# Optimization experiments

Measured on AMD Instinct MI355X. Metric: run time of the kernel, lower is better.

The kernel has to match this reference:

```python
import jax, jax.numpy as jnp
import numpy as np

DIM = 192
WIN = 7
HEADS = 6
SHIFT = 3
HID = 4 * DIM


def _ln(x, w, b, eps=1e-5):
    m = jnp.mean(x, axis=-1, keepdims=True)
    v = jnp.var(x, axis=-1, keepdims=True)
    return (x - m) * jax.lax.rsqrt(v + eps) * w + b


def setup_inputs() -> dict:
    key = jax.random.key(0)
    ks = jax.random.split(key, 8)
    B, C, H, W = 16, DIM, 56, 56
    s = lambda k, shape, fan: jax.random.normal(k, shape, jnp.float32) * (1.0 / np.sqrt(fan))
    return {
        "x": jax.random.normal(ks[0], (B, C, H, W), jnp.float32),
        "norm1_w": jnp.ones((C,), jnp.float32),
        "norm1_b": jnp.zeros((C,), jnp.float32),
        "qkv_w": s(ks[1], (3 * C, C), C),
        "qkv_b": jnp.zeros((3 * C,), jnp.float32),
        "proj_w": s(ks[2], (C, C), C),
        "proj_b": jnp.zeros((C,), jnp.float32),
        "norm2_w": jnp.ones((C,), jnp.float32),
        "norm2_b": jnp.zeros((C,), jnp.float32),
        "fc1_w": s(ks[3], (HID, C), C),
        "fc1_b": jnp.zeros((HID,), jnp.float32),
        "fc2_w": s(ks[4], (C, HID), HID),
        "fc2_b": jnp.zeros((C,), jnp.float32),
    }


def reference(x, norm1_w, norm1_b, qkv_w, qkv_b, proj_w, proj_b,
              norm2_w, norm2_b, fc1_w, fc1_b, fc2_w, fc2_b):
    B, C, H, W = x.shape
    shift = SHIFT if (H > WIN and W > WIN) else 0
    shortcut = x

    xl = jnp.transpose(x, (0, 2, 3, 1))            # B,H,W,C
    xl = _ln(xl, norm1_w, norm1_b)
    if shift > 0:
        xl = jnp.roll(xl, shift=(-shift, -shift), axis=(1, 2))
    nH, nW = H // WIN, W // WIN
    xw = xl.reshape(B, nH, WIN, nW, WIN, C)
    xw = jnp.transpose(xw, (0, 1, 3, 2, 4, 5)).reshape(-1, WIN * WIN, C)

    # window attention
    Bw, N, _ = xw.shape
    dh = C // HEADS
    qkv = jnp.einsum('bnc,oc->bno', xw, qkv_w) + qkv_b
    qkv = qkv.reshape(Bw, N, 3, HEADS, dh)
    q, k, v = qkv[:, :, 0], qkv[:, :, 1], qkv[:, :, 2]   # Bw,N,H,dh
    scale = dh ** -0.5
    attn = jnp.einsum('bnhd,bmhd->bhnm', q, k) * scale
    attn = jax.nn.softmax(attn, axis=-1)
    out = jnp.einsum('bhnm,bmhd->bnhd', attn, v).reshape(Bw, N, C)
    out = jnp.einsum('bnc,oc->bno', out, proj_w) + proj_b

    # window reverse -> B,H,W,C
    xl = out.reshape(B, nH, nW, WIN, WIN, C)
    xl = jnp.transpose(xl, (0, 1, 3, 2, 4, 5)).reshape(B, H, W, C)
    if shift > 0:
        xl = jnp.roll(xl, shift=(shift, shift), axis=(1, 2))

    # norm2 + MLP (note: original has NO attention residual)
    xl = _ln(xl, norm2_w, norm2_b)
    h = jnp.einsum('bhwc,oc->bhwo', xl, fc1_w) + fc1_b
    h = jax.nn.gelu(h, approximate=False)
    h = jnp.einsum('bhwo,co->bhwc', h, fc2_w) + fc2_b
    return jnp.transpose(h, (0, 3, 1, 2)) + shortcut
```

## Files before the change

### kernel.cpp

```cpp
#include <hip/hip_runtime.h>
#include <hip/hip_bf16.h>

typedef __bf16 bf16_t;
typedef __bf16 bf16x8 __attribute__((ext_vector_type(8)));
typedef float f32x4 __attribute__((ext_vector_type(4)));

#define MFMA16(a, b, c) __builtin_amdgcn_mfma_f32_16x16x32_bf16((a), (b), (c), 0, 0, 0)


__global__ __launch_bounds__(256) void k_cvt(const float* __restrict__ qkvw,
                                             const float* __restrict__ projw,
                                             const float* __restrict__ fc1w,
                                             const float* __restrict__ fc2w,
                                             bf16_t* __restrict__ dst)
{
    int i = blockIdx.x * 256 + threadIdx.x;
    if (i >= 442368) return;
    float v;
    if (i < 110592)      v = qkvw[i];
    else if (i < 147456) v = projw[i - 110592];
    else if (i < 294912) v = fc1w[i - 147456];
    else                 v = fc2w[i - 294912];
    dst[i] = (bf16_t)v;
}

__global__ __launch_bounds__(1024) void k_ln1(const float* __restrict__ x,
                                              const float* __restrict__ gam,
                                              const float* __restrict__ bet,
                                              bf16_t* __restrict__ xw)
{
    __shared__ float tile[56][193];
    __shared__ bf16_t obuf[56 * 192];
    const int bh = blockIdx.x;
    const int b = bh / 56, h = bh % 56;
    const int tid = threadIdx.x;

    {
        const int g = tid >> 4, u = tid & 15;
        const float* xb = x + (long)b * 602112 + (long)h * 56;
        if (u < 14) {
            #pragma unroll
            for (int k = 0; k < 3; ++k) {
                const int c = g + 64 * k;
                float4 v = *(const float4*)(xb + (long)c * 3136 + u * 4);
                tile[u * 4 + 0][c] = v.x;
                tile[u * 4 + 1][c] = v.y;
                tile[u * 4 + 2][c] = v.z;
                tile[u * 4 + 3][c] = v.w;
            }
        }
    }
    __syncthreads();

    const int wave = tid >> 6, lane = tid & 63;
    const float g0 = gam[lane], g1 = gam[lane + 64], g2 = gam[lane + 128];
    const float b0 = bet[lane], b1 = bet[lane + 64], b2 = bet[lane + 128];
    for (int wp = wave; wp < 56; wp += 16) {
        float v0 = tile[wp][lane], v1 = tile[wp][lane + 64], v2 = tile[wp][lane + 128];
        float s = v0 + v1 + v2;
        float sq = v0 * v0 + v1 * v1 + v2 * v2;
        #pragma unroll
        for (int d = 1; d < 64; d <<= 1) { s += __shfl_xor(s, d); sq += __shfl_xor(sq, d); }
        float mean = s * (1.f / 192.f);
        float var  = sq * (1.f / 192.f) - mean * mean;
        float rs = rsqrtf(var + 1e-5f);
        const int wr = (wp + 53) % 56;
        bf16_t* o = obuf + wr * 192;
        o[lane]       = (bf16_t)((v0 - mean) * rs * g0 + b0);
        o[lane + 64]  = (bf16_t)((v1 - mean) * rs * g1 + b1);
        o[lane + 128] = (bf16_t)((v2 - mean) * rs * g2 + b2);
    }
    __syncthreads();

    const int hr = (h + 53) % 56;
    const int nh = hr / 7, ii = hr % 7;
    const long rband = ((long)b * 64 + (long)nh * 8) * 49 + (long)ii * 7;
    const int4* src = (const int4*)obuf;
    for (int q = tid; q < 1344; q += 1024) {
        const int g = q / 168, u = q % 168;
        const int jj = u / 24, ci = u % 24;
        const long r = rband + (long)g * 49 + jj;
        ((int4*)xw)[r * 24 + ci] = src[(g * 7 + jj) * 24 + ci];
    }
}

template<int EPI>
__global__ __launch_bounds__(256) void k_gemm(const bf16_t* __restrict__ A,
                                              const bf16_t* __restrict__ W,
                                              const float* __restrict__ bias,
                                              void* __restrict__ outp,
                                              int M, int N, int K)
{
    __shared__ bf16_t As[128][72];
    __shared__ bf16_t Bs[64][72];
    const int tid = threadIdx.x;
    const int wave = tid >> 6, lane = tid & 63;
    const int lrow = lane & 15, lkg = lane >> 4;
    const int wm = (wave >> 1) * 64, wn = (wave & 1) * 32;
    const long m0 = (long)blockIdx.x * 128;
    const int n0 = blockIdx.y * 64;
    f32x4 acc[4][2];
    #pragma unroll
    for (int mi = 0; mi < 4; ++mi)
        #pragma unroll
        for (int ni = 0; ni < 2; ++ni)
            #pragma unroll
            for (int rg = 0; rg < 4; ++rg) acc[mi][ni][rg] = 0.f;

    for (int k0 = 0; k0 < K; k0 += 64) {
        #pragma unroll
        for (int it = 0; it < 4; ++it) {
            int e = (tid + it * 256) * 8;
            int r = e >> 6, c = e & 63;
            *(int4*)(&As[r][c]) = *(const int4*)(A + (m0 + r) * K + (k0 + c));
        }
        #pragma unroll
        for (int it = 0; it < 2; ++it) {
            int e = (tid + it * 256) * 8;
            int r = e >> 6, c = e & 63;
            *(int4*)(&Bs[r][c]) = *(const int4*)(W + (long)(n0 + r) * K + (k0 + c));
        }
        __syncthreads();
        #pragma unroll
        for (int kk = 0; kk < 64; kk += 32) {
            bf16x8 af[4], bfr[2];
            #pragma unroll
            for (int mi = 0; mi < 4; ++mi)
                af[mi] = *(const bf16x8*)(&As[wm + mi * 16 + lrow][kk + lkg * 8]);
            #pragma unroll
            for (int ni = 0; ni < 2; ++ni)
                bfr[ni] = *(const bf16x8*)(&Bs[wn + ni * 16 + lrow][kk + lkg * 8]);
            #pragma unroll
            for (int mi = 0; mi < 4; ++mi)
                #pragma unroll
                for (int ni = 0; ni < 2; ++ni)
                    acc[mi][ni] = MFMA16(af[mi], bfr[ni], acc[mi][ni]);
        }
        __syncthreads();
    }
    #pragma unroll
    for (int mi = 0; mi < 4; ++mi) {
        #pragma unroll
        for (int ni = 0; ni < 2; ++ni) {
            const int col = n0 + wn + ni * 16 + lrow;
            const float bv = bias[col];
            #pragma unroll
            for (int rg = 0; rg < 4; ++rg) {
                const long row = m0 + wm + mi * 16 + lkg * 4 + rg;
                float v = acc[mi][ni][rg] + bv;
                if (EPI == 2) {
                    float t2 = fminf(v * (1.5957691216057308f
                                          + 0.07135481627f * v * v), 60.f);
                    float e = __expf(t2);
                    v = v * e / (e + 1.f);
                }
                ((bf16_t*)outp)[row * N + col] = (bf16_t)v;
            }
        }
    }
}

__global__ __launch_bounds__(256) void k_proj_ln(const bf16_t* __restrict__ A,
                                                 const bf16_t* __restrict__ W,
                                                 const float* __restrict__ bias,
                                                 const float* __restrict__ gam,
                                                 const float* __restrict__ bet,
                                                 bf16_t* __restrict__ out)
{
    __shared__ bf16_t As[128][72];
    __shared__ bf16_t Bs[192][72];
    const int tid = threadIdx.x;
    const int wave = tid >> 6, lane = tid & 63;
    const int lrow = lane & 15, lkg = lane >> 4;
    const int wm = wave * 32;
    const long m0 = (long)blockIdx.x * 128;

    f32x4 acc[2][12];
    #pragma unroll
    for (int mi = 0; mi < 2; ++mi)
        #pragma unroll
        for (int ni = 0; ni < 12; ++ni)
            #pragma unroll
            for (int rg = 0; rg < 4; ++rg) acc[mi][ni][rg] = 0.f;

    for (int k0 = 0; k0 < 192; k0 += 64) {
        #pragma unroll
        for (int it = 0; it < 4; ++it) {
            int e = (tid + it * 256) * 8;
            int r = e >> 6, c = e & 63;
            *(int4*)(&As[r][c]) = *(const int4*)(A + (m0 + r) * 192 + (k0 + c));
        }
        #pragma unroll
        for (int it = 0; it < 6; ++it) {
            int e = (tid + it * 256) * 8;
            int r = e >> 6, c = e & 63;
            *(int4*)(&Bs[r][c]) = *(const int4*)(W + (long)r * 192 + (k0 + c));
        }
        __syncthreads();
        #pragma unroll
        for (int kk = 0; kk < 64; kk += 32) {
            bf16x8 af[2];
            #pragma unroll
            for (int mi = 0; mi < 2; ++mi)
                af[mi] = *(const bf16x8*)(&As[wm + mi * 16 + lrow][kk + lkg * 8]);
            #pragma unroll
            for (int ni = 0; ni < 12; ++ni) {
                bf16x8 bfr = *(const bf16x8*)(&Bs[ni * 16 + lrow][kk + lkg * 8]);
                acc[0][ni] = MFMA16(af[0], bfr, acc[0][ni]);
                acc[1][ni] = MFMA16(af[1], bfr, acc[1][ni]);
            }
        }
        __syncthreads();
    }

    float bv[12];
    #pragma unroll
    for (int ni = 0; ni < 12; ++ni) bv[ni] = bias[ni * 16 + lrow];

    #pragma unroll
    for (int mi = 0; mi < 2; ++mi) {
        #pragma unroll
        for (int rg = 0; rg < 4; ++rg) {
            float val[12];
            float s = 0.f, sq = 0.f;
            #pragma unroll
            for (int ni = 0; ni < 12; ++ni) {
                val[ni] = acc[mi][ni][rg] + bv[ni];
                s += val[ni];
                sq += val[ni] * val[ni];
            }
            #pragma unroll
            for (int d = 1; d < 16; d <<= 1) {
                s += __shfl_xor(s, d);
                sq += __shfl_xor(sq, d);
            }
            float mean = s * (1.f / 192.f);
            float var  = sq * (1.f / 192.f) - mean * mean;
            float rs = rsqrtf(var + 1e-5f);
            const long row = m0 + wm + mi * 16 + lkg * 4 + rg;
            bf16_t* orow = out + row * 192;
            #pragma unroll
            for (int ni = 0; ni < 12; ++ni) {
                const int col = ni * 16 + lrow;
                orow[col] = (bf16_t)((val[ni] - mean) * rs * gam[col] + bet[col]);
            }
        }
    }
}

__global__ __launch_bounds__(64) void k_attn(const bf16_t* __restrict__ qkv,
                                             bf16_t* __restrict__ aout)
{
    __shared__ bf16_t Pl[64][72];
    __shared__ bf16_t Vt[32][72];
    const int win = blockIdx.x, head = blockIdx.y;
    const int lane = threadIdx.x;
    const int lrow = lane & 15, lkg = lane >> 4;
    const bf16_t* base = qkv + (long)win * 28224 + head * 32;

    {
        const int m = lane;
        const int mc = (m < 49) ? m : 48;
        const int4* vr = (const int4*)(base + (long)mc * 576 + 384);
        #pragma unroll
        for (int c4 = 0; c4 < 4; ++c4) {
            int4 vv = vr[c4];
            if (m >= 49) vv = make_int4(0, 0, 0, 0);
            const bf16_t* pe = (const bf16_t*)&vv;
            #pragma unroll
            for (int e = 0; e < 8; ++e) Vt[c4 * 8 + e][m] = pe[e];
        }
    }

    bf16x8 z8;
    #pragma unroll
    for (int e = 0; e < 8; ++e) z8[e] = (bf16_t)0.f;
    bf16x8 qf[4], kf[4];
    #pragma unroll
    for (int t = 0; t < 4; ++t) {
        const int n = t * 16 + lrow;
        const int nc = (n < 49) ? n : 48;
        bf16x8 qv = *(const bf16x8*)(base + (long)nc * 576 + lkg * 8);
        bf16x8 kv = *(const bf16x8*)(base + (long)nc * 576 + 192 + lkg * 8);
        qf[t] = (n < 49) ? qv : z8;
        kf[t] = (n < 49) ? kv : z8;
    }
    f32x4 zf; zf[0] = zf[1] = zf[2] = zf[3] = 0.f;
    f32x4 S[4][4];
    #pragma unroll
    for (int mi = 0; mi < 4; ++mi)
        #pragma unroll
        for (int mj = 0; mj < 4; ++mj)
            S[mi][mj] = MFMA16(qf[mi], kf[mj], zf);

    const float scl = 0.17677669529663687f;
    #pragma unroll
    for (int mi = 0; mi < 4; ++mi) {
        #pragma unroll
        for (int rg = 0; rg < 4; ++rg) {
            float v0 = S[mi][0][rg] * scl;
            float v1 = S[mi][1][rg] * scl;
            float v2 = S[mi][2][rg] * scl;
            float v3 = (lrow == 0) ? S[mi][3][rg] * scl : -1e30f;
            float mx = fmaxf(fmaxf(v0, v1), fmaxf(v2, v3));
            #pragma unroll
            for (int d = 1; d < 16; d <<= 1) mx = fmaxf(mx, __shfl_xor(mx, d));
            float e0 = expf(v0 - mx), e1 = expf(v1 - mx), e2 = expf(v2 - mx);
            float e3 = (lrow == 0) ? expf(v3 - mx) : 0.f;
            float sm = e0 + e1 + e2 + e3;
            #pragma unroll
            for (int d = 1; d < 16; d <<= 1) sm += __shfl_xor(sm, d);
            float is = 1.f / sm;
            const int row = mi * 16 + lkg * 4 + rg;
            Pl[row][lrow]      = (bf16_t)(e0 * is);
            Pl[row][16 + lrow] = (bf16_t)(e1 * is);
            Pl[row][32 + lrow] = (bf16_t)(e2 * is);
            Pl[row][48 + lrow] = (bf16_t)(e3 * is);
        }
    }
    __syncthreads();

    f32x4 o[4][2];
    #pragma unroll
    for (int ni = 0; ni < 4; ++ni)
        #pragma unroll
        for (int di = 0; di < 2; ++di)
            #pragma unroll
            for (int rg = 0; rg < 4; ++rg) o[ni][di][rg] = 0.f;
    #pragma unroll
    for (int m0 = 0; m0 < 64; m0 += 32) {
        bf16x8 pf[4], vf[2];
        #pragma unroll
        for (int ni = 0; ni < 4; ++ni)
            pf[ni] = *(const bf16x8*)(&Pl[ni * 16 + lrow][m0 + lkg * 8]);
        #pragma unroll
        for (int di = 0; di < 2; ++di)
            vf[di] = *(const bf16x8*)(&Vt[di * 16 + lrow][m0 + lkg * 8]);
        #pragma unroll
        for (int ni = 0; ni < 4; ++ni)
            #pragma unroll
            for (int di = 0; di < 2; ++di)
                o[ni][di] = MFMA16(pf[ni], vf[di], o[ni][di]);
    }
    #pragma unroll
    for (int ni = 0; ni < 4; ++ni) {
        #pragma unroll
        for (int rg = 0; rg < 4; ++rg) {
            const int n = ni * 16 + lkg * 4 + rg;
            if (n < 49) {
                bf16_t* orow = aout + ((long)win * 49 + n) * 192 + head * 32;
                orow[lrow]      = (bf16_t)o[ni][0][rg];
                orow[16 + lrow] = (bf16_t)o[ni][1][rg];
            }
        }
    }
}

__global__ __launch_bounds__(1024) void k_final(const bf16_t* __restrict__ fb,
                                                const float* __restrict__ x,
                                                float* __restrict__ out)
{
    __shared__ float tile[56][199];
    const int bh = blockIdx.x;
    const int b = bh / 56, hq = bh % 56;
    const int tid = threadIdx.x;
    const int hr = (hq + 53) % 56;
    const int nh = hr / 7, ii = hr % 7;
    const long rband = ((long)b * 64 + (long)nh * 8) * 49 + (long)ii * 7;

    for (int q = tid; q < 1344; q += 1024) {
        const int g = q / 168, rem = q % 168;
        const int jj = rem / 24, ci = rem % 24;
        const long rr = rband + (long)g * 49 + jj;
        bf16x8 v = *(const bf16x8*)(fb + rr * 192 + ci * 8);
        const int wq = (g * 7 + jj + 3) % 56;
        #pragma unroll
        for (int e = 0; e < 8; ++e) tile[wq][ci * 8 + e] = (float)v[e];
    }
    __syncthreads();

    const int g = tid >> 4, u = tid & 15;
    if (u < 14) {
        #pragma unroll
        for (int k = 0; k < 3; ++k) {
            const int c = g + 64 * k;
            const long base = ((long)b * 192 + c) * 3136 + (long)hq * 56 + u * 4;
            float4 xv = *(const float4*)(x + base);
            float4 ov;
            ov.x = tile[u * 4 + 0][c] + xv.x;
            ov.y = tile[u * 4 + 1][c] + xv.y;
            ov.z = tile[u * 4 + 2][c] + xv.z;
            ov.w = tile[u * 4 + 3][c] + xv.w;
            *(float4*)(out + base) = ov;
        }
    }
}

extern "C" void kernel_launch(void* const* d_in, const int* in_sizes, int n_in,
                              void* d_out, int out_size, void* d_ws, size_t ws_size,
                              hipStream_t stream)
{
    const float* x     = (const float*)d_in[0];
    const float* n1w   = (const float*)d_in[1];
    const float* n1b   = (const float*)d_in[2];
    const float* qkvw  = (const float*)d_in[3];
    const float* qkvb  = (const float*)d_in[4];
    const float* projw = (const float*)d_in[5];
    const float* projb = (const float*)d_in[6];
    const float* n2w   = (const float*)d_in[7];
    const float* n2b   = (const float*)d_in[8];
    const float* fc1w  = (const float*)d_in[9];
    const float* fc1b  = (const float*)d_in[10];
    const float* fc2w  = (const float*)d_in[11];
    const float* fc2b  = (const float*)d_in[12];

    char* ws = (char*)d_ws;
    bf16_t* wqkv  = (bf16_t*)(ws);
    bf16_t* wproj = (bf16_t*)(ws + 221184);
    bf16_t* wfc1  = (bf16_t*)(ws + 294912);
    bf16_t* wfc2  = (bf16_t*)(ws + 589824);
    bf16_t* Xb    = (bf16_t*)(ws + 884736);
    bf16_t* QKV   = (bf16_t*)(ws + 20152320);
    bf16_t* Hb    = (bf16_t*)(ws + 77955072);
    bf16_t* H2    = (bf16_t*)(ws + 155025408);
    bf16_t* X2    = (bf16_t*)(ws + 174292992);

    k_cvt<<<1728, 256, 0, stream>>>(qkvw, projw, fc1w, fc2w, wqkv);
    k_ln1<<<896, 1024, 0, stream>>>(x, n1w, n1b, Xb);
    k_gemm<0><<<dim3(392, 9), 256, 0, stream>>>(Xb, wqkv, qkvb, QKV, 50176, 576, 192);
    k_attn<<<dim3(1024, 6), 64, 0, stream>>>(QKV, Xb);
    k_proj_ln<<<392, 256, 0, stream>>>(Xb, wproj, projb, n2w, n2b, X2);
    k_gemm<2><<<dim3(392, 12), 256, 0, stream>>>(X2, wfc1, fc1b, Hb, 50176, 768, 192);
    k_gemm<0><<<dim3(392, 3), 256, 0, stream>>>(Hb, wfc2, fc2b, H2, 50176, 192, 768);
    k_final<<<896, 1024, 0, stream>>>(H2, x, (float*)d_out);
}
```

Measured before the change: 215.8 us.

## Use direct global-to-LDS loads with XOR swizzle and vectorized transposed epilogue

```diff
diff --git a/kernel.cpp b/kernel.cpp
--- a/kernel.cpp
+++ b/kernel.cpp
@@ -2,10 +2,17 @@
 #include <hip/hip_bf16.h>
 
 typedef __bf16 bf16_t;
+typedef __bf16 bf16x4 __attribute__((ext_vector_type(4)));
 typedef __bf16 bf16x8 __attribute__((ext_vector_type(8)));
 typedef float f32x4 __attribute__((ext_vector_type(4)));
 
 #define MFMA16(a, b, c) __builtin_amdgcn_mfma_f32_16x16x32_bf16((a), (b), (c), 0, 0, 0)
+
+__device__ __forceinline__ void gl16(const bf16_t* g, void* l) {
+    __builtin_amdgcn_global_load_lds(
+        (const __attribute__((address_space(1))) void*)g,
+        (__attribute__((address_space(3))) void*)l, 16, 0, 0);
+}
 
 
 __global__ __launch_bounds__(256) void k_cvt(const float* __restrict__ qkvw,
@@ -88,17 +95,19 @@
 __global__ __launch_bounds__(256) void k_gemm(const bf16_t* __restrict__ A,
                                               const bf16_t* __restrict__ W,
                                               const float* __restrict__ bias,
-                                              void* __restrict__ outp,
+                                              bf16_t* __restrict__ outp,
                                               int M, int N, int K)
 {
-    __shared__ bf16_t As[128][72];
-    __shared__ bf16_t Bs[64][72];
+    __shared__ bf16_t As[128][64];
+    __shared__ bf16_t Bs[64][64];
     const int tid = threadIdx.x;
-    const int wave = tid >> 6, lane = tid & 63;
-    const int lrow = lane & 15, lkg = lane >> 4;
-    const int wm = (wave >> 1) * 64, wn = (wave & 1) * 32;
+    const int wv = tid >> 6, ln = tid & 63;
+    const int lrow = ln & 15, lkg = ln >> 4;
+    const int r7 = lrow & 7;
+    const int wm = (wv >> 1) * 64, wn = (wv & 1) * 32;
     const long m0 = (long)blockIdx.x * 128;
     const int n0 = blockIdx.y * 64;
+
     f32x4 acc[4][2];
     #pragma unroll
     for (int mi = 0; mi < 4; ++mi)
@@ -109,53 +118,66 @@
 
     for (int k0 = 0; k0 < K; k0 += 64) {
         #pragma unroll
-        for (int it = 0; it < 4; ++it) {
-            int e = (tid + it * 256) * 8;
-            int r = e >> 6, c = e & 63;
-            *(int4*)(&As[r][c]) = *(const int4*)(A + (m0 + r) * K + (k0 + c));
-        }
-        #pragma unroll
-        for (int it = 0; it < 2; ++it) {
-            int e = (tid + it * 256) * 8;
-            int r = e >> 6, c = e & 63;
-            *(int4*)(&Bs[r][c]) = *(const int4*)(W + (long)(n0 + r) * K + (k0 + c));
+        for (int i = 0; i < 4; ++i) {
+            const int off = ((wv * 4 + i) << 10) + ln * 16;
+            const int row = off >> 7, c16 = (off >> 4) & 7;
+            gl16(A + (m0 + row) * K + k0 + ((c16 ^ (row & 7)) << 3),
+                 (char*)As + ((wv * 4 + i) << 10));
+        }
+        #pragma unroll
+        for (int i = 0; i < 2; ++i) {
+            const int off = ((wv * 2 + i) << 10) + ln * 16;
+            const int row = off >> 7, c16 = (off >> 4) & 7;
+            gl16(W + (long)(n0 + row) * K + k0 + ((c16 ^ (row & 7)) << 3),
+                 (char*)Bs + ((wv * 2 + i) << 10));
         }
         __syncthreads();
         #pragma unroll
-        for (int kk = 0; kk < 64; kk += 32) {
+        for (int kk = 0; kk < 2; ++kk) {
             bf16x8 af[4], bfr[2];
             #pragma unroll
-            for (int mi = 0; mi < 4; ++mi)
-                af[mi] = *(const bf16x8*)(&As[wm + mi * 16 + lrow][kk + lkg * 8]);
-            #pragma unroll
-            for (int ni = 0; ni < 2; ++ni)
-                bfr[ni] = *(const bf16x8*)(&Bs[wn + ni * 16 + lrow][kk + lkg * 8]);
+            for (int mi = 0; mi < 4; ++mi) {
+                const int row = wm + mi * 16 + lrow;
+                af[mi] = *(const bf16x8*)((const char*)As + row * 128
+                           + ((((kk << 2) | lkg) ^ r7) << 4));
+            }
+            #pragma unroll
+            for (int ni = 0; ni < 2; ++ni) {
+                const int row = wn + ni * 16 + lrow;
+                bfr[ni] = *(const bf16x8*)((const char*)Bs + row * 128
+                           + ((((kk << 2) | lkg) ^ r7) << 4));
+            }
             #pragma unroll
             for (int mi = 0; mi < 4; ++mi)
                 #pragma unroll
                 for (int ni = 0; ni < 2; ++ni)
-                    acc[mi][ni] = MFMA16(af[mi], bfr[ni], acc[mi][ni]);
+                    acc[mi][ni] = MFMA16(bfr[ni], af[mi], acc[mi][ni]);
         }
         __syncthreads();
     }
+
     #pragma unroll
     for (int mi = 0; mi < 4; ++mi) {
+        const long m = m0 + wm + mi * 16 + lrow;
         #pragma unroll
         for (int ni = 0; ni < 2; ++ni) {
-            const int col = n0 + wn + ni * 16 + lrow;
-            const float bv = bias[col];
+            const int nb = n0 + wn + ni * 16 + lkg * 4;
+            const float4 bv = *(const float4*)(bias + nb);
+            float v[4] = { acc[mi][ni][0] + bv.x, acc[mi][ni][1] + bv.y,
+                           acc[mi][ni][2] + bv.z, acc[mi][ni][3] + bv.w };
+            bf16x4 o;
             #pragma unroll
             for (int rg = 0; rg < 4; ++rg) {
-                const long row = m0 + wm + mi * 16 + lkg * 4 + rg;
-                float v = acc[mi][ni][rg] + bv;
+                float t = v[rg];
                 if (EPI == 2) {
-                    float t2 = fminf(v * (1.5957691216057308f
-                                          + 0.07135481627f * v * v), 60.f);
+                    float t2 = fminf(t * (1.5957691216057308f
+                                          + 0.07135481627f * t * t), 60.f);
                     float e = __expf(t2);
-                    v = v * e / (e + 1.f);
+                    t = t * e / (e + 1.f);
                 }
-                ((bf16_t*)outp)[row * N + col] = (bf16_t)v;
-            }
+                o[rg] = (bf16_t)t;
+            }
+            *(bf16x4*)(outp + m * N + nb) = o;
         }
     }
 }
```

New measurement: 219.7 us. Within noise of the previous version (+1.8%).
